# Performance work log

Hardware: AMD Instinct MI355X
Metric: run time of the kernel (lower is better)

## Reference

```python
import jax, jax.numpy as jnp
import numpy as np

DIM = 1024
NUM_HEADS = 16
HEAD_DIM = DIM // NUM_HEADS
MAX_LEN = 2048
ROPE_BASE = 10000.0


def _rope_tables(n, d, base=ROPE_BASE):
    inv_freq = 1.0 / (base ** (np.arange(0, d, 2, dtype=np.float32) / d))  # [d/2]
    t = np.arange(n, dtype=np.float32)
    freqs = np.outer(t, inv_freq)  # [n, d/2]
    return jnp.asarray(np.cos(freqs)), jnp.asarray(np.sin(freqs))


def _apply_rotary(x, cos, sin):
    # x: [B, H, N, D]; pairs are consecutive elements (2i, 2i+1)
    xe = x[..., 0::2]
    xo = x[..., 1::2]
    # cos/sin: [N, D/2] -> broadcast over B, H
    oe = xe * cos - xo * sin
    oo = xe * sin + xo * cos
    return jnp.stack([oe, oo], axis=-1).reshape(x.shape)


def setup_inputs() -> dict:
    key = jax.random.key(0)
    ks = jax.random.split(key, 11)
    B, T, S = 4, 2048, 2048
    sc = 1.0 / np.sqrt(DIM)
    inp = {
        "query": jax.random.normal(ks[0], (B, T, DIM), jnp.float32),
        "key": jax.random.normal(ks[1], (B, S, DIM), jnp.float32),
        "value": jax.random.normal(ks[2], (B, S, DIM), jnp.float32),
        "Wq": jax.random.normal(ks[3], (DIM, DIM), jnp.float32) * sc,
        "bq": jnp.zeros((DIM,), jnp.float32),
        "Wk": jax.random.normal(ks[4], (DIM, DIM), jnp.float32) * sc,
        "bk": jnp.zeros((DIM,), jnp.float32),
        "Wv": jax.random.normal(ks[5], (DIM, DIM), jnp.float32) * sc,
        "bv": jnp.zeros((DIM,), jnp.float32),
        "Wo": jax.random.normal(ks[6], (DIM, DIM), jnp.float32) * sc,
        "bo": jnp.zeros((DIM,), jnp.float32),
    }
    return inp


def reference(query, key, value, Wq, bq, Wk, bk, Wv, bv, Wo, bo):
    B, T, C = query.shape
    S = key.shape[1]
    H, D = NUM_HEADS, HEAD_DIM
    scale = D ** -0.5

    q = (query @ Wq + bq).reshape(B, T, H, D).transpose(0, 2, 1, 3)  # [B,H,T,D]
    k = (key @ Wk + bk).reshape(B, S, H, D).transpose(0, 2, 1, 3)    # [B,H,S,D]
    v = (value @ Wv + bv).reshape(B, S, H, D).transpose(0, 2, 1, 3)  # [B,H,S,D]

    cos, sin = _rope_tables(max(T, S), D)
    q = _apply_rotary(q, cos[:T], sin[:T])
    k = _apply_rotary(k, cos[:S], sin[:S])

    scores = jnp.einsum("bhtd,bhsd->bhts", q, k) * scale  # [B,H,T,S]
    causal = jnp.tril(jnp.ones((T, S), bool))
    scores = jnp.where(causal[None, None], scores, -jnp.inf)
    att = jax.nn.softmax(scores, axis=-1)

    out = jnp.einsum("bhts,bhsd->bhtd", att, v)  # [B,H,T,D]
    out = out.transpose(0, 2, 1, 3).reshape(B, T, C)
    return out @ Wo + bo
```

## Files before the change

kernel.cpp:

```cpp
#include <hip/hip_runtime.h>
#include <cstdint>
#include <math.h>

typedef __bf16 bf16_t;
typedef __bf16 bf16x8 __attribute__((ext_vector_type(8)));
typedef __bf16 bf16x4 __attribute__((ext_vector_type(4)));
typedef float f32x4 __attribute__((ext_vector_type(4)));

#define MFMA16(a, b, c) __builtin_amdgcn_mfma_f32_16x16x32_bf16((a), (b), (c), 0, 0, 0)

static constexpr int BATCH = 4;
static constexpr int SEQ = 2048;
static constexpr int DIMC = 1024;
static constexpr int NH = 16;
static constexpr int HD = 64;

__device__ __forceinline__ void async_copy16(void* lds, const void* g) {
    __builtin_amdgcn_global_load_lds(
        (const __attribute__((address_space(1))) void*)g,
        (__attribute__((address_space(3))) void*)lds, 16, 0, 0);
}

__device__ __forceinline__ float fast_exp2(float x) {
#if __has_builtin(__builtin_amdgcn_exp2f)
    return __builtin_amdgcn_exp2f(x);
#else
    return __expf(x * 0.6931471805599453f);
#endif
}

__global__ __launch_bounds__(256) void cvt3(const float* __restrict__ q,
                                            const float* __restrict__ k,
                                            const float* __restrict__ v,
                                            bf16_t* __restrict__ out) {
    const float* in = (blockIdx.y == 0) ? q : ((blockIdx.y == 1) ? k : v);
    bf16_t* o = out + (size_t)blockIdx.y * BATCH * SEQ * DIMC;
    const int i = blockIdx.x * 256 + threadIdx.x;
    const float4 f0 = ((const float4*)in)[i * 2];
    const float4 f1 = ((const float4*)in)[i * 2 + 1];
    bf16x8 vv;
    vv[0] = (bf16_t)f0.x; vv[1] = (bf16_t)f0.y; vv[2] = (bf16_t)f0.z; vv[3] = (bf16_t)f0.w;
    vv[4] = (bf16_t)f1.x; vv[5] = (bf16_t)f1.y; vv[6] = (bf16_t)f1.z; vv[7] = (bf16_t)f1.w;
    ((bf16x8*)o)[i] = vv;
}

__global__ __launch_bounds__(256) void transpose_cvt(const float* __restrict__ W0,
                                                     const float* __restrict__ W1,
                                                     const float* __restrict__ W2,
                                                     const float* __restrict__ W3,
                                                     bf16_t* __restrict__ out) {
    const float* Ws[4] = {W0, W1, W2, W3};
    const float* W = Ws[blockIdx.z];
    bf16_t* Wt = out + (size_t)blockIdx.z * DIMC * DIMC;
    __shared__ float tile[32][33];
    const int tx = threadIdx.x & 31;
    const int ty = threadIdx.x >> 5;
    const int x0 = blockIdx.x * 32;
    const int y0 = blockIdx.y * 32;
    #pragma unroll
    for (int j = ty; j < 32; j += 8)
        tile[j][tx] = W[(size_t)(y0 + j) * DIMC + x0 + tx];
    __syncthreads();
    #pragma unroll
    for (int j = ty; j < 32; j += 8)
        Wt[(size_t)(x0 + j) * DIMC + y0 + tx] = (bf16_t)tile[tx][j];
}

__global__ __launch_bounds__(256) void rope_tab(float* __restrict__ cosT, float* __restrict__ sinT) {
    const int idx = blockIdx.x * 256 + threadIdx.x;
    const int t = idx >> 5;
    const int p = idx & 31;
    const float inv = exp2f(-0.41524101186092029f * (float)p);
    const float ang = (float)t * inv;
    float s, c;
    sincosf(ang, &s, &c);
    cosT[idx] = c;
    sinT[idx] = s;
}

#define GEMM_KLOOP(A_, Bt_)                                                             \
    f32x4 acc[4][4] = {};                                                               \
    const int swW = ((lane >> 2) & 3) ^ ((lane >> 4) & 3);         \
    const int rIn = lane >> 2;                                    \
    const int gW = ((lane & 3) ^ swW) * 8;                        \
    const int fR = (l15 & 3) ^ ((l15 >> 2) & 3);                    \
    for (int kt = 0; kt < DIMC / 32; ++kt) {                                            \
        const int k0 = kt * 32;                                                         \
        __syncthreads();                                                                \
        _Pragma("unroll") for (int ci = 0; ci < 2; ++ci) {                              \
            const int c = 2 * w + ci;                                                   \
            async_copy16(&Bs[c * 512], Bt_ + (size_t)(col0 + c * 16 + rIn) * DIMC + k0 + gW); \
            async_copy16(&As[c * 512], A_ + (size_t)(row0 + c * 16 + rIn) * DIMC + k0 + gW);  \
        }                                                                               \
        __syncthreads();                                                                \
        bf16x8 af[4], bfr[4];                                                           \
        _Pragma("unroll") for (int mt = 0; mt < 4; ++mt)                                \
            af[mt] = *(const bf16x8*)&As[(wr * 64 + mt * 16 + l15) * 32 + ((quad ^ fR) << 3)]; \
        _Pragma("unroll") for (int nt = 0; nt < 4; ++nt)                                \
            bfr[nt] = *(const bf16x8*)&Bs[(wc * 64 + nt * 16 + l15) * 32 + ((quad ^ fR) << 3)]; \
        _Pragma("unroll") for (int mt = 0; mt < 4; ++mt)                                \
            _Pragma("unroll") for (int nt = 0; nt < 4; ++nt)                            \
                acc[mt][nt] = MFMA16(af[mt], bfr[nt], acc[mt][nt]);                     \
    }

__global__ __launch_bounds__(256) void gemm_qkv(const bf16_t* __restrict__ Cb,
                                                const bf16_t* __restrict__ Wt3,
                                                const float* __restrict__ bq,
                                                const float* __restrict__ bk,
                                                const float* __restrict__ bv,
                                                bf16_t* __restrict__ Qr,
                                                bf16_t* __restrict__ Kr,
                                                bf16_t* __restrict__ Vr,
                                                const float* __restrict__ cosT,
                                                const float* __restrict__ sinT) {
    __shared__ __align__(16) unsigned char smem[32 * 132 * 4];
    bf16_t* As = (bf16_t*)smem;
    bf16_t* Bs = (bf16_t*)(smem + 8192);
    float* eps = (float*)smem;
    const int z = blockIdx.z;
    const bf16_t* A = Cb + (size_t)z * BATCH * SEQ * DIMC;
    const bf16_t* Bt = Wt3 + (size_t)z * DIMC * DIMC;
    const float* bias = (z == 0) ? bq : ((z == 1) ? bk : bv);
    bf16_t* outp = (z == 0) ? Qr : ((z == 1) ? Kr : Vr);
    const bool rope = (z < 2);
    const int tid = threadIdx.x;
    const int w = tid >> 6;
    const int lane = tid & 63;
    const int l15 = lane & 15;
    const int quad = lane >> 4;
    const int wr = w >> 1, wc = w & 1;
    const int raw = blockIdx.y * 8 + blockIdx.x;
    const int row0 = (raw & 63) * 128, col0 = (raw >> 6) * 128;
    GEMM_KLOOP(A, Bt)
    float bvl[4];
    #pragma unroll
    for (int nt = 0; nt < 4; ++nt) bvl[nt] = bias[col0 + wc * 64 + nt * 16 + l15];
    const int lr = tid >> 3;
    const int cg = tid & 7;
    const int c0 = cg * 16;
    const int h = (col0 + c0) >> 6;
    const int dbase = (col0 + c0) & 63;
    #pragma unroll
    for (int p = 0; p < 4; ++p) {
        __syncthreads();
        #pragma unroll
        for (int nt = 0; nt < 4; ++nt)
            #pragma unroll
            for (int r = 0; r < 4; ++r)
                eps[(wr * 16 + quad * 4 + r) * 132 + wc * 64 + nt * 16 + l15] =
                    acc[p][nt][r] + bvl[nt];
        __syncthreads();
        const int grow = row0 + (lr >> 4) * 64 + p * 16 + (lr & 15);
        const int t = grow & (SEQ - 1);
        const int bb = grow >> 11;
        float vals[16];
        #pragma unroll
        for (int q4 = 0; q4 < 4; ++q4) {
            f32x4 vv = *(const f32x4*)&eps[lr * 132 + c0 + q4 * 4];
            vals[q4 * 4 + 0] = vv[0]; vals[q4 * 4 + 1] = vv[1];
            vals[q4 * 4 + 2] = vv[2]; vals[q4 * 4 + 3] = vv[3];
        }
        bf16x8 o0, o1;
        if (rope) {
            const float osc = (z == 0) ? 0.18033688011112043f : 1.0f;
            const int pbase = t * 32 + (dbase >> 1);
            const float4 cs0 = *(const float4*)&cosT[pbase];
            const float4 cs1 = *(const float4*)&cosT[pbase + 4];
            const float4 sn0 = *(const float4*)&sinT[pbase];
            const float4 sn1 = *(const float4*)&sinT[pbase + 4];
            const float cc[8] = {cs0.x, cs0.y, cs0.z, cs0.w, cs1.x, cs1.y, cs1.z, cs1.w};
            const float ss[8] = {sn0.x, sn0.y, sn0.z, sn0.w, sn1.x, sn1.y, sn1.z, sn1.w};
            #pragma unroll
            for (int i = 0; i < 8; ++i) {
                const float e = vals[2 * i], o = vals[2 * i + 1];
                const float oe = (e * cc[i] - o * ss[i]) * osc;
                const float oo = (e * ss[i] + o * cc[i]) * osc;
                if (i < 4) { o0[2 * i] = (bf16_t)oe; o0[2 * i + 1] = (bf16_t)oo; }
                else { o1[2 * (i - 4)] = (bf16_t)oe; o1[2 * (i - 4) + 1] = (bf16_t)oo; }
            }
        } else {
            #pragma unroll
            for (int i = 0; i < 8; ++i) o0[i] = (bf16_t)vals[i];
            #pragma unroll
            for (int i = 0; i < 8; ++i) o1[i] = (bf16_t)vals[8 + i];
        }
        bf16_t* dst = outp + (((size_t)bb * NH + h) * SEQ + t) * HD + dbase;
        *(bf16x8*)dst = o0;
        *(bf16x8*)(dst + 8) = o1;
    }
}

__global__ __launch_bounds__(256) void gemm_o(const bf16_t* __restrict__ A,
                                              const bf16_t* __restrict__ Bt,
                                              const float* __restrict__ bias,
                                              float* __restrict__ out) {
    __shared__ __align__(16) unsigned char smem[16384];
    bf16_t* As = (bf16_t*)smem;
    bf16_t* Bs = (bf16_t*)(smem + 8192);
    const int tid = threadIdx.x;
    const int w = tid >> 6;
    const int lane = tid & 63;
    const int l15 = lane & 15;
    const int quad = lane >> 4;
    const int wr = w >> 1, wc = w & 1;
    const int raw = blockIdx.y * 8 + blockIdx.x;
    const int row0 = (raw & 63) * 128, col0 = (raw >> 6) * 128;
    GEMM_KLOOP(A, Bt)
    #pragma unroll
    for (int nt = 0; nt < 4; ++nt) {
        const int col = col0 + wc * 64 + nt * 16 + l15;
        const float bvl = bias[col];
        #pragma unroll
        for (int mt = 0; mt < 4; ++mt) {
            #pragma unroll
            for (int r = 0; r < 4; ++r) {
                const int row = row0 + wr * 64 + mt * 16 + quad * 4 + r;
                out[(size_t)row * DIMC + col] = acc[mt][nt][r] + bvl;
            }
        }
    }
}

__global__ __launch_bounds__(256) void attn_kernel(const bf16_t* __restrict__ Qr,
                                                   const bf16_t* __restrict__ Kr,
                                                   const bf16_t* __restrict__ Vr,
                                                   bf16_t* __restrict__ O) {
    __shared__ bf16_t Ks[2][64 * 64];
    __shared__ bf16_t Vt[2][64 * 72];
    __shared__ bf16_t Ps[4][32 * 72];
    const int tid = threadIdx.x;
    const int w = tid >> 6;
    const int lane = tid & 63;
    const int l15 = lane & 15;
    const int quad = lane >> 4;
    const int bh = blockIdx.x;
    const int b = bh >> 4, h = bh & 15;
    const bf16_t* Qb = Qr + (size_t)bh * SEQ * HD;
    const bf16_t* Kb = Kr + (size_t)bh * SEQ * HD;
    const bf16_t* Vb = Vr + (size_t)bh * SEQ * HD;

    bf16x8 ones;
    #pragma unroll
    for (int j8 = 0; j8 < 8; ++j8) ones[j8] = (bf16_t)1.0f;
    bf16x8 idB[2];
    #pragma unroll
    for (int ch = 0; ch < 2; ++ch)
        #pragma unroll
        for (int j8 = 0; j8 < 8; ++j8)
            idB[ch][j8] = (quad * 8 + j8 == ch * 16 + l15) ? (bf16_t)1.0f : (bf16_t)0.0f;

    const int sIn = lane >> 3;
    const int gK = ((lane & 7) ^ sIn) * 8;
    const int fK = (l15 & 7);

#define VTRANS(buf, a0, a1)                                                      \
    {                                                                            \
        _Pragma("unroll") for (int c = 0; c < 4; ++c) {                          \
            f32x4 zt = {};                                                       \
            f32x4 tv = MFMA16((c < 2) ? (a0) : (a1), idB[c & 1], zt);            \
            bf16x4 pkt;                                                          \
            _Pragma("unroll") for (int rr = 0; rr < 4; ++rr)                     \
                pkt[rr] = (bf16_t)tv[rr];                                        \
            *(bf16x4*)&Vt[buf][(c * 16 + l15) * 72 + w * 16 + quad * 4] = pkt;   \
        }                                                                        \
    }

    const int j = 15 - (int)blockIdx.y;
    const int q0 = j * 128;
    bf16x8 qa[2][2];
    #pragma unroll
    for (int mg = 0; mg < 2; ++mg)
        #pragma unroll
        for (int kc = 0; kc < 2; ++kc)
            qa[mg][kc] = *(const bf16x8*)(Qb + (size_t)(q0 + mg * 64 + w * 16 + l15) * HD +
                                          kc * 32 + quad * 8);
    f32x4 acco[2][4] = {};
    f32x4 accl[2] = {};
    const int nIter = 2 * j + 2;

    #pragma unroll
    for (int ci = 0; ci < 2; ++ci) {
        const int c = 2 * w + ci;
        async_copy16(&Ks[0][c * 512], Kb + (size_t)(c * 8 + sIn) * HD + gK);
    }
    {
        const bf16_t* vsrc = Vb + (size_t)(w * 16 + l15) * HD + quad * 8;
        bf16x8 pv0 = *(const bf16x8*)vsrc;
        bf16x8 pv1 = *(const bf16x8*)(vsrc + 32);
        VTRANS(0, pv0, pv1);
    }
    __syncthreads();

    int cur = 0;
    for (int it = 0; it < nIter; ++it) {
        const int nxt = cur ^ 1;
        const bool hn = (it + 1 < nIter);
        bf16x8 av0, av1;
        if (hn) {
            const int s1 = (it + 1) * 64;
            #pragma unroll
            for (int ci = 0; ci < 2; ++ci) {
                const int c = 2 * w + ci;
                async_copy16(&Ks[nxt][c * 512], Kb + (size_t)(s1 + c * 8 + sIn) * HD + gK);
            }
            const bf16_t* vsrc = Vb + (size_t)(s1 + w * 16 + l15) * HD + quad * 8;
            av0 = *(const bf16x8*)vsrc;
            av1 = *(const bf16x8*)(vsrc + 32);
        }
        bf16x8 kb[4][2];
        #pragma unroll
        for (int mt = 0; mt < 4; ++mt)
            #pragma unroll
            for (int kc = 0; kc < 2; ++kc)
                kb[mt][kc] = *(const bf16x8*)&Ks[cur][(mt * 16 + l15) * 64 +
                                                      (((kc * 4 + quad) ^ fK) << 3)];
        const bool skip0 = (it == 2 * j + 1);
        f32x4 zz[2][4];
        __builtin_amdgcn_s_setprio(1);
        #pragma unroll
        for (int mg = 0; mg < 2; ++mg) {
            if (mg == 0 && skip0) continue;
            #pragma unroll
            for (int mt = 0; mt < 4; ++mt) {
                f32x4 z = {};
                z = MFMA16(kb[mt][0], qa[mg][0], z);
                z = MFMA16(kb[mt][1], qa[mg][1], z);
                zz[mg][mt] = z;
            }
        }
        __builtin_amdgcn_s_setprio(0);
        #pragma unroll
        for (int mg = 0; mg < 2; ++mg) {
            if (mg == 0 && skip0) continue;
            const bool diag = (it == 2 * j + mg);
            #pragma unroll
            for (int mt = 0; mt < 4; ++mt) {
                bf16x4 pk;
                #pragma unroll
                for (int r = 0; r < 4; ++r) {
                    float v = zz[mg][mt][r];
                    if (diag && (mt * 16 + quad * 4 + r > w * 16 + l15)) v = -INFINITY;
                    pk[r] = (bf16_t)fast_exp2(v);
                }
                *(bf16x4*)&Ps[w][(mg * 16 + l15) * 72 + mt * 16 + quad * 4] = pk;
            }
        }
        asm volatile("s_waitcnt lgkmcnt(0)" ::: "memory");
        bf16x8 vb[4][2];
        #pragma unroll
        for (int dt = 0; dt < 4; ++dt)
            #pragma unroll
            for (int kc = 0; kc < 2; ++kc)
                vb[dt][kc] = *(const bf16x8*)&Vt[cur][(dt * 16 + l15) * 72 + kc * 32 + quad * 8];
        #pragma unroll
        for (int mg = 0; mg < 2; ++mg) {
            if (mg == 0 && skip0) continue;
            const bf16x8 pa0 = *(const bf16x8*)&Ps[w][(mg * 16 + l15) * 72 + quad * 8];
            const bf16x8 pa1 = *(const bf16x8*)&Ps[w][(mg * 16 + l15) * 72 + 32 + quad * 8];
            __builtin_amdgcn_s_setprio(1);
            #pragma unroll
            for (int dt = 0; dt < 4; ++dt) {
                acco[mg][dt] = MFMA16(pa0, vb[dt][0], acco[mg][dt]);
                acco[mg][dt] = MFMA16(pa1, vb[dt][1], acco[mg][dt]);
            }
            accl[mg] = MFMA16(pa0, ones, accl[mg]);
            accl[mg] = MFMA16(pa1, ones, accl[mg]);
            __builtin_amdgcn_s_setprio(0);
        }
        if (hn) VTRANS(nxt, av0, av1);
        __syncthreads();
        cur = nxt;
    }
    #pragma unroll
    for (int mg = 0; mg < 2; ++mg) {
        #pragma unroll
        for (int r = 0; r < 4; ++r) {
            const float inv = 1.0f / accl[mg][r];
            const int trow = q0 + mg * 64 + w * 16 + quad * 4 + r;
            bf16_t* orow = O + ((size_t)(b * SEQ + trow)) * DIMC + h * HD;
            #pragma unroll
            for (int dt = 0; dt < 4; ++dt)
                orow[dt * 16 + l15] = (bf16_t)(acco[mg][dt][r] * inv);
        }
    }
#undef VTRANS
}

extern "C" void kernel_launch(void* const* d_in, const int* in_sizes, int n_in,
                              void* d_out, int out_size, void* d_ws, size_t ws_size,
                              hipStream_t stream) {
    const float* query = (const float*)d_in[0];
    const float* key = (const float*)d_in[1];
    const float* value = (const float*)d_in[2];
    const float* Wq = (const float*)d_in[3];
    const float* bq = (const float*)d_in[4];
    const float* Wk = (const float*)d_in[5];
    const float* bk = (const float*)d_in[6];
    const float* Wv = (const float*)d_in[7];
    const float* bv = (const float*)d_in[8];
    const float* Wo = (const float*)d_in[9];
    const float* bo = (const float*)d_in[10];

    char* ws = (char*)d_ws;
    const size_t WT_BYTES = (size_t)DIMC * DIMC * sizeof(bf16_t);
    const size_t ACT_BYTES = (size_t)BATCH * SEQ * DIMC * sizeof(bf16_t);
    bf16_t* WT = (bf16_t*)ws;
    bf16_t* WoT = WT + 3 * (size_t)DIMC * DIMC;
    float* cosT = (float*)(ws + 4 * WT_BYTES);
    float* sinT = (float*)(ws + 4 * WT_BYTES + 262144);
    bf16_t* Cb = (bf16_t*)(ws + 4 * WT_BYTES + 2 * 262144);
    bf16_t* Qr = (bf16_t*)((char*)Cb + 3 * ACT_BYTES);
    bf16_t* Kr = (bf16_t*)((char*)Cb + 4 * ACT_BYTES);
    bf16_t* Vr = (bf16_t*)((char*)Cb + 5 * ACT_BYTES);
    bf16_t* Ob = Cb;

    transpose_cvt<<<dim3(32, 32, 4), 256, 0, stream>>>(Wq, Wk, Wv, Wo, WT);
    rope_tab<<<dim3(256), 256, 0, stream>>>(cosT, sinT);
    cvt3<<<dim3(4096, 3), 256, 0, stream>>>(query, key, value, Cb);
    gemm_qkv<<<dim3(DIMC / 128, (BATCH * SEQ) / 128, 3), 256, 0, stream>>>(
        Cb, WT, bq, bk, bv, Qr, Kr, Vr, cosT, sinT);
    attn_kernel<<<dim3(BATCH * NH, 16), 256, 0, stream>>>(Qr, Kr, Vr, Ob);
    gemm_o<<<dim3(DIMC / 128, (BATCH * SEQ) / 128), 256, 0, stream>>>(Ob, WoT, bo, (float*)d_out);
}
```

Before: 334.9 us.

## Triple-buffer GEMM k-loop with async LDS loads and larger 512-thread tiles

Replaces the single-buffered GEMM macro with a templated core that keeps three LDS stages in flight. It waits with explicit vmcnt counts and a single barrier per k-step, so global-to-LDS copies overlap the MFMA work. QKV tiles grow to 256x256 and output-projection tiles to 128x256 with 512-thread blocks, and MFMA issue gets raised priority. This cuts the sync overhead and load latency exposed by the old two-barrier loop, at the cost of much more LDS per block, more registers, and fewer blocks in the grid.

Measured after the change: 332.5 us. No clear change (-0.7%).

```diff
diff --git a/kernel.cpp b/kernel.cpp
--- a/kernel.cpp
+++ b/kernel.cpp
@@ -78,44 +78,101 @@
     sinT[idx] = s;
 }
 
-#define GEMM_KLOOP(A_, Bt_)                                                             \
-    f32x4 acc[4][4] = {};                                                               \
-    const int swW = ((lane >> 2) & 3) ^ ((lane >> 4) & 3);         \
-    const int rIn = lane >> 2;                                    \
-    const int gW = ((lane & 3) ^ swW) * 8;                        \
-    const int fR = (l15 & 3) ^ ((l15 >> 2) & 3);                    \
-    for (int kt = 0; kt < DIMC / 32; ++kt) {                                            \
-        const int k0 = kt * 32;                                                         \
-        __syncthreads();                                                                \
+template <int MI>
+__device__ __forceinline__ void gemm_core(const bf16_t* __restrict__ A,
+                                          const bf16_t* __restrict__ Bt,
+                                          const int row0, const int col0,
+                                          bf16_t* As, bf16_t* Bs, const int tid,
+                                          f32x4 (&acc)[MI][4]) {
+    constexpr int ABUF = MI * 32 * 32;
+    constexpr int BBUF = 256 * 32;
+    constexpr int NT = DIMC / 32;
+    const int wid = tid >> 6;
+    const int lane = tid & 63;
+    const int l15 = lane & 15;
+    const int quad = lane >> 4;
+    const int wr = wid >> 2;
+    const int wc = wid & 3;
+    const int rIn = lane >> 2;
+    const int gW = ((lane & 3) ^ ((rIn & 3) ^ ((rIn >> 2) & 3))) * 8;
+    const int fR = (l15 & 3) ^ ((l15 >> 2) & 3);
+
+#define STAGE_TILE(bi, kt)                                                              \
+    {                                                                                   \
+        const int k0_ = (kt)*32;                                                        \
+        bf16_t* as_ = As + (bi)*ABUF;                                                   \
+        bf16_t* bs_ = Bs + (bi)*BBUF;                                                   \
+        if constexpr (MI == 8) {                                                        \
+            _Pragma("unroll") for (int ci = 0; ci < 2; ++ci) {                          \
+                const int c = 2 * wid + ci;                                             \
+                async_copy16(&as_[c * 512],                                             \
+                             A + (size_t)(row0 + c * 16 + rIn) * DIMC + k0_ + gW);      \
+            }                                                                           \
+        } else {                                                                        \
+            async_copy16(&as_[wid * 512],                                               \
+                         A + (size_t)(row0 + wid * 16 + rIn) * DIMC + k0_ + gW);        \
+        }                                                                               \
         _Pragma("unroll") for (int ci = 0; ci < 2; ++ci) {                              \
-            const int c = 2 * w + ci;                                                   \
-            async_copy16(&Bs[c * 512], Bt_ + (size_t)(col0 + c * 16 + rIn) * DIMC + k0 + gW); \
-            async_copy16(&As[c * 512], A_ + (size_t)(row0 + c * 16 + rIn) * DIMC + k0 + gW);  \
+            const int c = 2 * wid + ci;                                                 \
+            async_copy16(&bs_[c * 512],                                                 \
+                         Bt + (size_t)(col0 + c * 16 + rIn) * DIMC + k0_ + gW);         \
         }                                                                               \
-        __syncthreads();                                                                \
-        bf16x8 af[4], bfr[4];                                                           \
-        _Pragma("unroll") for (int mt = 0; mt < 4; ++mt)                                \
-            af[mt] = *(const bf16x8*)&As[(wr * 64 + mt * 16 + l15) * 32 + ((quad ^ fR) << 3)]; \
-        _Pragma("unroll") for (int nt = 0; nt < 4; ++nt)                                \
-            bfr[nt] = *(const bf16x8*)&Bs[(wc * 64 + nt * 16 + l15) * 32 + ((quad ^ fR) << 3)]; \
-        _Pragma("unroll") for (int mt = 0; mt < 4; ++mt)                                \
-            _Pragma("unroll") for (int nt = 0; nt < 4; ++nt)                            \
-                acc[mt][nt] = MFMA16(af[mt], bfr[nt], acc[mt][nt]);                     \
-    }
-
-__global__ __launch_bounds__(256) void gemm_qkv(const bf16_t* __restrict__ Cb,
-                                                const bf16_t* __restrict__ Wt3,
-                                                const float* __restrict__ bq,
-                                                const float* __restrict__ bk,
-                                                const float* __restrict__ bv,
-                                                bf16_t* __restrict__ Qr,
-                                                bf16_t* __restrict__ Kr,
-                                                bf16_t* __restrict__ Vr,
-                                                const float* __restrict__ cosT,
-                                                const float* __restrict__ sinT) {
-    __shared__ __align__(16) unsigned char smem[32 * 132 * 4];
+    }
+
+    STAGE_TILE(0, 0)
+    STAGE_TILE(1, 1)
+    int rb = 0;
+    for (int t = 0; t < NT; ++t) {
+        if (t == NT - 1) {
+            asm volatile("s_waitcnt vmcnt(0)" ::: "memory");
+        } else {
+            if constexpr (MI == 8)
+                asm volatile("s_waitcnt vmcnt(4)" ::: "memory");
+            else
+                asm volatile("s_waitcnt vmcnt(3)" ::: "memory");
+        }
+        asm volatile("s_barrier" ::: "memory");
+        if (t + 2 < NT) {
+            int sb = rb + 2;
+            if (sb >= 3) sb -= 3;
+            STAGE_TILE(sb, t + 2)
+        }
+        const bf16_t* as = As + rb * ABUF;
+        const bf16_t* bs = Bs + rb * BBUF;
+        bf16x8 bfrag[4];
+        #pragma unroll
+        for (int ni = 0; ni < 4; ++ni)
+            bfrag[ni] = *(const bf16x8*)&bs[(wc * 64 + ni * 16 + l15) * 32 + ((quad ^ fR) << 3)];
+        bf16x8 afrag[MI];
+        #pragma unroll
+        for (int mi = 0; mi < MI; ++mi)
+            afrag[mi] =
+                *(const bf16x8*)&as[(wr * (MI * 16) + mi * 16 + l15) * 32 + ((quad ^ fR) << 3)];
+        __builtin_amdgcn_s_setprio(1);
+        #pragma unroll
+        for (int mi = 0; mi < MI; ++mi)
+            #pragma unroll
+            for (int ni = 0; ni < 4; ++ni)
+                acc[mi][ni] = MFMA16(afrag[mi], bfrag[ni], acc[mi][ni]);
+        __builtin_amdgcn_s_setprio(0);
+        rb = rb + 1 == 3 ? 0 : rb + 1;
+    }
+#undef STAGE_TILE
+}
+
+__global__ __launch_bounds__(512, 2) void gemm_qkv(const bf16_t* __restrict__ Cb,
+                                                   const bf16_t* __restrict__ Wt3,
+                                                   const float* __restrict__ bq,
+                                                   const float* __restrict__ bk,
+                                                   const float* __restrict__ bv,
+                                                   bf16_t* __restrict__ Qr,
+                                                   bf16_t* __restrict__ Kr,
+                                                   bf16_t* __restrict__ Vr,
+                                                   const float* __restrict__ cosT,
+                                                   const float* __restrict__ sinT) {
+    __shared__ __align__(16) unsigned char smem[98304];
     bf16_t* As = (bf16_t*)smem;
-    bf16_t* Bs = (bf16_t*)(smem + 8192);
+    bf16_t* Bs = (bf16_t*)(smem + 49152);
     float* eps = (float*)smem;
     const int z = blockIdx.z;
     const bf16_t* A = Cb + (size_t)z * BATCH * SEQ * DIMC;
@@ -124,46 +181,47 @@
     bf16_t* outp = (z == 0) ? Qr : ((z == 1) ? Kr : Vr);
     const bool rope = (z < 2);
     const int tid = threadIdx.x;
-    const int w = tid >> 6;
+    const int row0 = blockIdx.y * 256, col0 = blockIdx.x * 256;
+    f32x4 acc[8][4] = {};
+    gemm_core<8>(A, Bt, row0, col0, As, Bs, tid, acc);
+
+    const int wid = tid >> 6;
     const int lane = tid & 63;
     const int l15 = lane & 15;
     const int quad = lane >> 4;
-    const int wr = w >> 1, wc = w & 1;
-    const int raw = blockIdx.y * 8 + blockIdx.x;
-    const int row0 = (raw & 63) * 128, col0 = (raw >> 6) * 128;
-    GEMM_KLOOP(A, Bt)
+    const int wr = wid >> 2, wc = wid & 3;
     float bvl[4];
     #pragma unroll
-    for (int nt = 0; nt < 4; ++nt) bvl[nt] = bias[col0 + wc * 64 + nt * 16 + l15];
-    const int lr = tid >> 3;
-    const int cg = tid & 7;
+    for (int ni = 0; ni < 4; ++ni) bvl[ni] = bias[col0 + wc * 64 + ni * 16 + l15];
+    const int lr = tid >> 4;
+    const int cg = tid & 15;
     const int c0 = cg * 16;
     const int h = (col0 + c0) >> 6;
-    const int dbase = (col0 + c0) & 63;
-    #pragma unroll
-    for (int p = 0; p < 4; ++p) {
+    const int dbase = c0 & 63;
+    const float osc = (z == 0) ? 0.18033688011112043f : 1.0f;
+    #pragma unroll
+    for (int p = 0; p < 8; ++p) {
         __syncthreads();
         #pragma unroll
-        for (int nt = 0; nt < 4; ++nt)
+        for (int ni = 0; ni < 4; ++ni)
             #pragma unroll
             for (int r = 0; r < 4; ++r)
-                eps[(wr * 16 + quad * 4 + r) * 132 + wc * 64 + nt * 16 + l15] =
-                    acc[p][nt][r] + bvl[nt];
+                eps[(wr * 16 + quad * 4 + r) * 264 + wc * 64 + ni * 16 + l15] =
+                    acc[p][ni][r] + bvl[ni];
         __syncthreads();
-        const int grow = row0 + (lr >> 4) * 64 + p * 16 + (lr & 15);
-        const int t = grow & (SEQ - 1);
+        const int grow = row0 + (lr >> 4) * 128 + p * 16 + (lr & 15);
+        const int tq = grow & (SEQ - 1);
         const int bb = grow >> 11;
         float vals[16];
         #pragma unroll
         for (int q4 = 0; q4 < 4; ++q4) {
-            f32x4 vv = *(const f32x4*)&eps[lr * 132 + c0 + q4 * 4];
+            f32x4 vv = *(const f32x4*)&eps[lr * 264 + c0 + q4 * 4];
             vals[q4 * 4 + 0] = vv[0]; vals[q4 * 4 + 1] = vv[1];
             vals[q4 * 4 + 2] = vv[2]; vals[q4 * 4 + 3] = vv[3];
         }
         bf16x8 o0, o1;
         if (rope) {
-            const float osc = (z == 0) ? 0.18033688011112043f : 1.0f;
-            const int pbase = t * 32 + (dbase >> 1);
+            const int pbase = tq * 32 + (dbase >> 1);
             const float4 cs0 = *(const float4*)&cosT[pbase];
             const float4 cs1 = *(const float4*)&cosT[pbase + 4];
             const float4 sn0 = *(const float4*)&sinT[pbase];
@@ -184,38 +242,38 @@
             #pragma unroll
             for (int i = 0; i < 8; ++i) o1[i] = (bf16_t)vals[8 + i];
         }
-        bf16_t* dst = outp + (((size_t)bb * NH + h) * SEQ + t) * HD + dbase;
+        bf16_t* dst = outp + (((size_t)bb * NH + h) * SEQ + tq) * HD + dbase;
         *(bf16x8*)dst = o0;
         *(bf16x8*)(dst + 8) = o1;
     }
 }
 
-__global__ __launch_bounds__(256) void gemm_o(const bf16_t* __restrict__ A,
-                                              const bf16_t* __restrict__ Bt,
-                                              const float* __restrict__ bias,
-                                              float* __restrict__ out) {
-    __shared__ __align__(16) unsigned char smem[16384];
+__global__ __launch_bounds__(512, 2) void gemm_o(const bf16_t* __restrict__ A,
+                                                 const bf16_t* __restrict__ Bt,
+                                                 const float* __restrict__ bias,
+                                                 float* __restrict__ out) {
+    __shared__ __align__(16) unsigned char smem[73728];
     bf16_t* As = (bf16_t*)smem;
-    bf16_t* Bs = (bf16_t*)(smem + 8192);
+    bf16_t* Bs = (bf16_t*)(smem + 24576);
     const int tid = threadIdx.x;
-    const int w = tid >> 6;
+    const int row0 = blockIdx.y * 128, col0 = blockIdx.x * 256;
+    f32x4 acc[4][4] = {};
+    gemm_core<4>(A, Bt, row0, col0, As, Bs, tid, acc);
+    const int wid = tid >> 6;
     const int lane = tid & 63;
     const int l15 = lane & 15;
     const int quad = lane >> 4;
-    const int wr = w >> 1, wc = w & 1;
-    const int raw = blockIdx.y * 8 + blockIdx.x;
-    const int row0 = (raw & 63) * 128, col0 = (raw >> 6) * 128;
-    GEMM_KLOOP(A, Bt)
-    #pragma unroll
-    for (int nt = 0; nt < 4; ++nt) {
-        const int col = col0 + wc * 64 + nt * 16 + l15;
+    const int wr = wid >> 2, wc = wid & 3;
+    #pragma unroll
+    for (int ni = 0; ni < 4; ++ni) {
+        const int col = col0 + wc * 64 + ni * 16 + l15;
         const float bvl = bias[col];
         #pragma unroll
-        for (int mt = 0; mt < 4; ++mt) {
+        for (int mi = 0; mi < 4; ++mi) {
             #pragma unroll
             for (int r = 0; r < 4; ++r) {
-                const int row = row0 + wr * 64 + mt * 16 + quad * 4 + r;
-                out[(size_t)row * DIMC + col] = acc[mt][nt][r] + bvl;
+                const int row = row0 + wr * 64 + mi * 16 + quad * 4 + r;
+                out[(size_t)row * DIMC + col] = acc[mi][ni][r] + bvl;
             }
         }
     }
@@ -417,8 +475,8 @@
     transpose_cvt<<<dim3(32, 32, 4), 256, 0, stream>>>(Wq, Wk, Wv, Wo, WT);
     rope_tab<<<dim3(256), 256, 0, stream>>>(cosT, sinT);
     cvt3<<<dim3(4096, 3), 256, 0, stream>>>(query, key, value, Cb);
-    gemm_qkv<<<dim3(DIMC / 128, (BATCH * SEQ) / 128, 3), 256, 0, stream>>>(
+    gemm_qkv<<<dim3(DIMC / 256, (BATCH * SEQ) / 256, 3), 512, 0, stream>>>(
         Cb, WT, bq, bk, bv, Qr, Kr, Vr, cosT, sinT);
     attn_kernel<<<dim3(BATCH * NH, 16), 256, 0, stream>>>(Qr, Kr, Vr, Ob);
-    gemm_o<<<dim3(DIMC / 128, (BATCH * SEQ) / 128), 256, 0, stream>>>(Ob, WoT, bo, (float*)d_out);
-}
+    gemm_o<<<dim3(DIMC / 256, (BATCH * SEQ) / 128), 512, 0, stream>>>(Ob, WoT, bo, (float*)d_out);
+}
```
